# Kernel optimization log

Hardware: AMD Instinct MI355X
Metric: run time of the kernel (lower is better)

## Reference

```python
import jax, jax.numpy as jnp
import numpy as np

N = 50000; E = 800000; B = 500; L = 42
F_IN = 35; HEADS = 10; F_H = 35; F_G = 350
VOCAB = 26; EMB = 128; NF = 16; OUT_DIM = 128; K = 8
NEG_SLOPE = 0.2


def setup_inputs() -> dict:
    key = jax.random.key(0)
    ks = jax.random.split(key, 16)
    inp = {}
    inp['x'] = jax.random.normal(ks[0], (N, F_IN), jnp.float32)
    inp['edge_index'] = jax.random.randint(ks[1], (2, E), 0, N, dtype=jnp.int32)
    inp['batch'] = jnp.sort(jax.random.randint(ks[2], (N,), 0, B, dtype=jnp.int32))
    inp['target'] = jax.random.randint(ks[3], (B, L), 0, VOCAB, dtype=jnp.int32)
    # --- learned parameters ---
    inp['W_gat'] = jax.random.normal(ks[4], (F_IN, HEADS * F_H), jnp.float32) * 0.1
    inp['att_src'] = jax.random.normal(ks[5], (HEADS, F_H), jnp.float32) * 0.1
    inp['att_dst'] = jax.random.normal(ks[6], (HEADS, F_H), jnp.float32) * 0.1
    inp['b_gat'] = jnp.zeros((HEADS * F_H,), jnp.float32)
    inp['W_gcn'] = jax.random.normal(ks[7], (F_G, F_G), jnp.float32) * 0.05
    inp['b_gcn'] = jnp.zeros((F_G,), jnp.float32)
    inp['W_fcg1'] = jax.random.normal(ks[8], (2 * F_G, 1500), jnp.float32) * 0.03
    inp['b_fcg1'] = jnp.zeros((1500,), jnp.float32)
    inp['W_fcg2'] = jax.random.normal(ks[9], (1500, OUT_DIM), jnp.float32) * 0.03
    inp['b_fcg2'] = jnp.zeros((OUT_DIM,), jnp.float32)
    inp['emb_xt'] = jax.random.normal(ks[10], (VOCAB, EMB), jnp.float32) * 0.1
    inp['W_conv'] = jax.random.normal(ks[11], (NF, EMB, K), jnp.float32) * 0.05
    inp['b_conv'] = jnp.zeros((NF,), jnp.float32)
    inp['W_fcxt'] = jax.random.normal(ks[12], (NF * 35, OUT_DIM), jnp.float32) * 0.05
    inp['b_fcxt'] = jnp.zeros((OUT_DIM,), jnp.float32)
    inp['W_fc1'] = jax.random.normal(ks[13], (256, 512), jnp.float32) * 0.05
    inp['b_fc1'] = jnp.zeros((512,), jnp.float32)
    inp['W_out'] = jax.random.normal(ks[14], (512, 1), jnp.float32) * 0.05
    inp['b_out'] = jnp.zeros((1,), jnp.float32)
    return inp


def _add_self_loops(edge_index):
    loop = jnp.arange(N, dtype=edge_index.dtype)
    src = jnp.concatenate([edge_index[0], loop])
    dst = jnp.concatenate([edge_index[1], loop])
    return src, dst


def _gat_conv(x, src, dst, W, att_src, att_dst, b):
    # h: [N, H, C]
    h = (x @ W).reshape(N, HEADS, F_H)
    a_s = jnp.einsum('nhc,hc->nh', h, att_src)  # [N, H]
    a_d = jnp.einsum('nhc,hc->nh', h, att_dst)
    e = jax.nn.leaky_relu(a_s[src] + a_d[dst], NEG_SLOPE)  # [Etot, H]
    # segment softmax over incoming edges per destination node, per head
    m = jax.ops.segment_max(e, dst, num_segments=N)
    m = jnp.where(jnp.isfinite(m), m, 0.0)
    ex = jnp.exp(e - m[dst])
    den = jax.ops.segment_sum(ex, dst, num_segments=N)
    alpha = ex / (den[dst] + 1e-16)  # [Etot, H]
    out = jax.ops.segment_sum(h[src] * alpha[:, :, None], dst, num_segments=N)
    return out.reshape(N, HEADS * F_H) + b, alpha


def _gcn_conv(x, src, dst, W, b):
    deg = jax.ops.segment_sum(jnp.ones_like(dst, jnp.float32), dst, num_segments=N)
    dinv = jnp.where(deg > 0, deg ** -0.5, 0.0)
    norm = dinv[src] * dinv[dst]  # symmetric normalization
    h = x @ W
    return jax.ops.segment_sum(h[src] * norm[:, None], dst, num_segments=N) + b


def reference(x, edge_index, batch, target, W_gat, att_src, att_dst, b_gat,
              W_gcn, b_gcn, W_fcg1, b_fcg1, W_fcg2, b_fcg2, emb_xt,
              W_conv, b_conv, W_fcxt, b_fcxt, W_fc1, b_fc1, W_out, b_out):
    src, dst = _add_self_loops(edge_index)
    # --- graph branch ---
    xg, alpha = _gat_conv(x, src, dst, W_gat, att_src, att_dst, b_gat)
    xg = jax.nn.relu(xg)
    xg = jax.nn.relu(_gcn_conv(xg, src, dst, W_gcn, b_gcn))
    # global max + mean pool per graph
    gmax = jax.ops.segment_max(xg, batch, num_segments=B)
    gsum = jax.ops.segment_sum(xg, batch, num_segments=B)
    cnt = jax.ops.segment_sum(jnp.ones((N,), jnp.float32), batch, num_segments=B)
    gmean = gsum / jnp.maximum(cnt, 1.0)[:, None]
    xg = jnp.concatenate([gmax, gmean], axis=1)  # [B, 700]
    xg = jax.nn.relu(xg @ W_fcg1 + b_fcg1)
    xg = xg @ W_fcg2 + b_fcg2  # [B, 128] (dropout is identity in eval)
    # --- protein branch ---
    emb = emb_xt[target]                      # [B, L, 128]
    emb = jnp.transpose(emb, (0, 2, 1))       # [B, 128, L]
    conv = jax.lax.conv_general_dilated(
        emb, W_conv, window_strides=(1,), padding='VALID',
        dimension_numbers=('NCH', 'OIH', 'NCH'))  # [B, 16, 35]
    conv = conv + b_conv[None, :, None]
    xt = conv.reshape(B, NF * 35)
    xt = xt @ W_fcxt + b_fcxt                 # [B, 128]
    # --- fusion ---
    xc = jnp.concatenate([xg, xt], axis=1)    # [B, 256]
    xc = jax.nn.relu(xc @ W_fc1 + b_fc1)
    out = jax.nn.sigmoid(xc @ W_out + b_out)  # [B, 1]
    return out, alpha
```

## Files before the change

### kernel.cpp

```cpp
#include <hip/hip_runtime.h>
#include <math.h>

#define NN 50000
#define EE 800000
#define BB 500
#define LL 42
#define NHEAD 10
#define FH 35
#define FG 350
#define ETOT (EE + NN)
#define NCHUNK ((NN + 511) / 512)

#define KPAD 384
#define MPAD 50048
#define MB2  512

typedef unsigned short ushort_t;
typedef __attribute__((ext_vector_type(8))) short short8v;
typedef __attribute__((ext_vector_type(4))) float float4v;

__device__ __forceinline__ float lrelu(float x) { return x > 0.f ? x : 0.2f * x; }

__device__ __forceinline__ ushort_t f2bf(float f) {
    unsigned int u = __float_as_uint(f);
    u += 0x7fffu + ((u >> 16) & 1u);
    return (ushort_t)(u >> 16);
}
__device__ __forceinline__ float bflo(unsigned u) { return __uint_as_float(u << 16); }
__device__ __forceinline__ float bfhi(unsigned u) { return __uint_as_float(u & 0xffff0000u); }
__device__ __forceinline__ unsigned packbf(float a, float b) {
    return (unsigned)f2bf(a) | ((unsigned)f2bf(b) << 16);
}

__device__ __forceinline__ void async_cp16(const void* g, void* l) {
    __builtin_amdgcn_global_load_lds((const __attribute__((address_space(1))) unsigned int*)g,
                                     (__attribute__((address_space(3))) unsigned int*)l, 16, 0, 0);
}

__global__ __launch_bounds__(256) void k_init(int* deg, int* cur) {
    int i = blockIdx.x * 256 + threadIdx.x;
    if (i < NN) { deg[i] = 1; cur[i] = 0; }
}

__global__ __launch_bounds__(256) void k_deg(const int* __restrict__ ei, int* deg) {
    int i = blockIdx.x * 256 + threadIdx.x;
    if (i < EE) atomicAdd(&deg[ei[EE + i]], 1);
}

__global__ __launch_bounds__(512) void k_scan1(const int* __restrict__ deg, int* part) {
    int i = blockIdx.x * 512 + threadIdx.x;
    int lane = threadIdx.x & 63, wv = threadIdx.x >> 6;
    int x = (i < NN) ? deg[i] : 0;
    #pragma unroll
    for (int d = 32; d; d >>= 1) x += __shfl_xor(x, d);
    __shared__ int wsum[8];
    if (lane == 0) wsum[wv] = x;
    __syncthreads();
    if (threadIdx.x == 0) {
        int s = 0;
        #pragma unroll
        for (int w = 0; w < 8; w++) s += wsum[w];
        part[blockIdx.x] = s;
    }
}

__global__ __launch_bounds__(64) void k_scan2(const int* __restrict__ part, int* pscan) {
    int l = threadIdx.x;
    int v0 = (l < NCHUNK) ? part[l] : 0;
    #pragma unroll
    for (int d = 1; d < 64; d <<= 1) { int t = __shfl_up(v0, d); if (l >= d) v0 += t; }
    int tot0 = __shfl(v0, 63);
    int v1 = (64 + l < NCHUNK) ? part[64 + l] : 0;
    #pragma unroll
    for (int d = 1; d < 64; d <<= 1) { int t = __shfl_up(v1, d); if (l >= d) v1 += t; }
    v1 += tot0;
    if (l < NCHUNK) pscan[l] = v0;
    if (64 + l < NCHUNK) pscan[64 + l] = v1;
}

__global__ __launch_bounds__(512) void k_scan3(const int* __restrict__ deg, const int* __restrict__ pscan,
                                               int* offs) {
    int i = blockIdx.x * 512 + threadIdx.x;
    int lane = threadIdx.x & 63, wv = threadIdx.x >> 6;
    int x = (i < NN) ? deg[i] : 0;
    int incl = x;
    #pragma unroll
    for (int d = 1; d < 64; d <<= 1) { int t = __shfl_up(incl, d); if (lane >= d) incl += t; }
    __shared__ int wtot[8];
    if (lane == 63) wtot[wv] = incl;
    __syncthreads();
    int woff = 0;
    for (int w = 0; w < wv; w++) woff += wtot[w];
    int base = (blockIdx.x == 0) ? 0 : pscan[blockIdx.x - 1];
    if (i < NN) offs[i] = base + woff + incl - x;
}

__global__ __launch_bounds__(256) void k_scatter(const int* __restrict__ ei, const int* __restrict__ offs,
                                                 int* cur, int* csr_src) {
    int i = blockIdx.x * 256 + threadIdx.x;
    if (i < EE) {
        int s = ei[i], d = ei[EE + i];
        int slot = atomicAdd(&cur[d], 1);
        csr_src[offs[d] + slot] = s;
    } else if (i < ETOT) {
        int v = i - EE;
        int slot = atomicAdd(&cur[v], 1);
        csr_src[offs[v] + slot] = v;
    }
}

__global__ __launch_bounds__(256) void k_dinv(const int* __restrict__ deg, float* dinv) {
    int i = blockIdx.x * 256 + threadIdx.x;
    if (i < NN) dinv[i] = rsqrtf((float)deg[i]);
}

__global__ __launch_bounds__(256) void k_prep_x(const float* __restrict__ x, ushort_t* __restrict__ xb) {
    int i = blockIdx.x * 256 + threadIdx.x;
    if (i >= MPAD * 64) return;
    int r = i / 64, k = i % 64;
    float v = (r < NN && k < 35) ? x[r * 35 + k] : 0.f;
    xb[i] = f2bf(v);
}

__global__ __launch_bounds__(256) void k_prep_wgat(const float* __restrict__ W, ushort_t* __restrict__ Wt) {
    int i = blockIdx.x * 256 + threadIdx.x;
    if (i >= KPAD * 64) return;
    int n = i / 64, k = i % 64;
    float v = (n < FG && k < 35) ? W[k * FG + n] : 0.f;
    Wt[i] = f2bf(v);
}

__global__ __launch_bounds__(256) void k_prep_wgcn(const float* __restrict__ W, ushort_t* __restrict__ Wt) {
    int i = blockIdx.x * 256 + threadIdx.x;
    if (i >= KPAD * KPAD) return;
    int n = i / KPAD, k = i % KPAD;
    float v = (n < FG && k < FG) ? W[k * FG + n] : 0.f;
    Wt[i] = f2bf(v);
}

__global__ __launch_bounds__(256) void k_prep_w(const float* __restrict__ W, ushort_t* __restrict__ Wt,
                                                int K, int N, int KP, int NP) {
    int i = blockIdx.x * 256 + threadIdx.x;
    if (i >= KP * NP) return;
    int k = i / NP, n = i % NP;
    float v = (k < K && n < N) ? W[(size_t)k * N + n] : 0.f;
    Wt[(size_t)n * KP + k] = f2bf(v);
}

__global__ __launch_bounds__(256) void k_cast_pad(const float* __restrict__ src, ushort_t* __restrict__ dst,
                                                  int M, int K, int MP, int KP) {
    int i = blockIdx.x * 256 + threadIdx.x;
    if (i >= MP * KP) return;
    int r = i / KP, k = i % KP;
    dst[i] = (r < M && k < K) ? f2bf(src[(size_t)r * K + k]) : (ushort_t)0;
}

__global__ __launch_bounds__(256) void k_zero_tail(ushort_t* xg1b) {
    int i = blockIdx.x * 256 + threadIdx.x;
    int total = (MPAD - NN) * KPAD;
    if (i < total) xg1b[(size_t)NN * KPAD + i] = 0;
}

__global__ __launch_bounds__(256) void k_mfma(const ushort_t* __restrict__ A, const ushort_t* __restrict__ Bt,
                                              void* __restrict__ C, int M, int Nv, int ldc, int lda,
                                              int ksteps, const float* __restrict__ bias, int act, int bf16out) {
    __shared__ ushort_t As[128 * 64];
    __shared__ ushort_t Bs[64 * 64];
    int tid = threadIdx.x;
    int wid = tid >> 6, lane = tid & 63;
    int m0 = blockIdx.y * 128, n0 = blockIdx.x * 64;
    int wm0 = (wid >> 1) * 64, wn0 = (wid & 1) * 32;
    int srow = tid >> 3;
    int scol = (tid & 7) * 8;
    float4v acc[4][2] = {{{0.f,0.f,0.f,0.f},{0.f,0.f,0.f,0.f}},
                         {{0.f,0.f,0.f,0.f},{0.f,0.f,0.f,0.f}},
                         {{0.f,0.f,0.f,0.f},{0.f,0.f,0.f,0.f}},
                         {{0.f,0.f,0.f,0.f},{0.f,0.f,0.f,0.f}}};
    int a_off = (wm0 + (lane & 15)) * 64 + (lane >> 4) * 8;
    int b_off = (wn0 + (lane & 15)) * 64 + (lane >> 4) * 8;
    for (int ks = 0; ks < ksteps; ks++) {
        int k0 = ks * 64;
        #pragma unroll
        for (int r = 0; r < 4; r++) {
            const ushort_t* g = A + (size_t)(m0 + r * 32 + srow) * lda + k0 + scol;
            async_cp16(g, As + (r * 256 + tid) * 8);
        }
        #pragma unroll
        for (int r = 0; r < 2; r++) {
            const ushort_t* g = Bt + (size_t)(n0 + r * 32 + srow) * lda + k0 + scol;
            async_cp16(g, Bs + (r * 256 + tid) * 8);
        }
        __syncthreads();
        #pragma unroll
        for (int kh = 0; kh < 2; kh++) {
            short8v b0 = *(const short8v*)&Bs[b_off + kh * 32];
            short8v b1 = *(const short8v*)&Bs[b_off + 16 * 64 + kh * 32];
            #pragma unroll
            for (int mi = 0; mi < 4; mi++) {
                short8v a = *(const short8v*)&As[a_off + mi * 16 * 64 + kh * 32];
                acc[mi][0] = __builtin_amdgcn_mfma_f32_16x16x32_bf16(a, b0, acc[mi][0], 0, 0, 0);
                acc[mi][1] = __builtin_amdgcn_mfma_f32_16x16x32_bf16(a, b1, acc[mi][1], 0, 0, 0);
            }
        }
        __syncthreads();
    }
    int lm = m0 + wm0 + (lane >> 4) * 4;
    int lc = n0 + wn0 + (lane & 15);
    #pragma unroll
    for (int mi = 0; mi < 4; mi++) {
        #pragma unroll
        for (int ni = 0; ni < 2; ni++) {
            int col = lc + ni * 16;
            float bv = (bias != nullptr && col < Nv) ? bias[col] : 0.f;
            #pragma unroll
            for (int r = 0; r < 4; r++) {
                int row = lm + mi * 16 + r;
                if (row >= M) continue;
                float v = acc[mi][ni][r] + bv;
                if (act) v = fmaxf(v, 0.f);
                if (col >= Nv) v = 0.f;
                if (bf16out) ((ushort_t*)C)[(size_t)row * ldc + col] = f2bf(v);
                else         ((float*)C)[(size_t)row * ldc + col] = v;
            }
        }
    }
}

__global__ __launch_bounds__(256) void k_att(const ushort_t* __restrict__ hb, const float* __restrict__ att_s,
                                             const float* __restrict__ att_d, float* __restrict__ a_s,
                                             float* __restrict__ a_d) {
    int tid = blockIdx.x * 256 + threadIdx.x;
    if (tid >= NN * NHEAD) return;
    int n = tid / NHEAD, hd = tid % NHEAD;
    const ushort_t* hr = hb + (size_t)n * KPAD + hd * FH;
    const float* ws = att_s + hd * FH;
    const float* wd = att_d + hd * FH;
    float as = 0.f, ad = 0.f;
    #pragma unroll
    for (int c = 0; c < FH; c++) {
        float v = __uint_as_float(((unsigned)hr[c]) << 16);
        as += v * ws[c]; ad += v * wd[c];
    }
    a_s[tid] = as;
    a_d[tid] = ad;
}

__global__ __launch_bounds__(256) void k_gat_agg(const ushort_t* __restrict__ hb, const float* __restrict__ a_s,
                                                 const float* __restrict__ a_d,
                                                 const int* __restrict__ csr_src,
                                                 const int* __restrict__ offs, const int* __restrict__ deg,
                                                 const float* __restrict__ b_gat,
                                                 ushort_t* __restrict__ xg1b, float* __restrict__ denArr) {
    int wid = (blockIdx.x * blockDim.x + threadIdx.x) >> 6;
    int lane = threadIdx.x & 63;
    if (wid >= NN) return;
    int o0 = offs[wid], d = deg[wid];
    bool mine = (lane < NHEAD);
    float adv = mine ? a_d[wid * NHEAD + lane] : 0.f;
    int hA0 = (2 * lane) / 35,       hA1 = (2 * lane + 1) / 35;
    int hB0 = (128 + 2 * lane) / 35, hB1 = (129 + 2 * lane) / 35;
    int hC0 = (256 + 2 * lane) / 35, hC1 = (257 + 2 * lane) / 35;
    float den = 0.f;
    float aL0 = 0.f, aH0 = 0.f, aL1 = 0.f, aH1 = 0.f, aL2 = 0.f, aH2 = 0.f;
    const unsigned* hb32 = (const unsigned*)hb;
    int i = 0;
    for (; i + 2 <= d; i += 2) {
        int s0 = csr_src[o0 + i], s1 = csr_src[o0 + i + 1];
        float as0 = mine ? a_s[s0 * NHEAD + lane] : 0.f;
        float as1 = mine ? a_s[s1 * NHEAD + lane] : 0.f;
        const unsigned* h0 = hb32 + (size_t)s0 * (KPAD / 2);
        const unsigned* h1 = hb32 + (size_t)s1 * (KPAD / 2);
        unsigned u00 = h0[lane], u01 = h0[lane + 64], u02 = h0[lane + 128];
        unsigned u10 = h1[lane], u11 = h1[lane + 64], u12 = h1[lane + 128];
        float ex0 = __expf(lrelu(as0 + adv));
        float ex1 = __expf(lrelu(as1 + adv));
        den += ex0 + ex1;
        aL0 += __shfl(ex0, hA0) * bflo(u00) + __shfl(ex1, hA0) * bflo(u10);
        aH0 += __shfl(ex0, hA1) * bfhi(u00) + __shfl(ex1, hA1) * bfhi(u10);
        aL1 += __shfl(ex0, hB0) * bflo(u01) + __shfl(ex1, hB0) * bflo(u11);
        aH1 += __shfl(ex0, hB1) * bfhi(u01) + __shfl(ex1, hB1) * bfhi(u11);
        aL2 += __shfl(ex0, hC0) * bflo(u02) + __shfl(ex1, hC0) * bflo(u12);
        aH2 += __shfl(ex0, hC1) * bfhi(u02) + __shfl(ex1, hC1) * bfhi(u12);
    }
    for (; i < d; i++) {
        int s = csr_src[o0 + i];
        float asv = mine ? a_s[s * NHEAD + lane] : 0.f;
        float ex = __expf(lrelu(asv + adv));
        den += ex;
        const unsigned* hr = hb32 + (size_t)s * (KPAD / 2);
        unsigned u0 = hr[lane], u1 = hr[lane + 64], u2 = hr[lane + 128];
        aL0 += __shfl(ex, hA0) * bflo(u0);  aH0 += __shfl(ex, hA1) * bfhi(u0);
        aL1 += __shfl(ex, hB0) * bflo(u1);  aH1 += __shfl(ex, hB1) * bfhi(u1);
        aL2 += __shfl(ex, hC0) * bflo(u2);  aH2 += __shfl(ex, hC1) * bfhi(u2);
    }
    float rden = 1.f / (den + 1e-16f);
    if (mine) denArr[wid * NHEAD + lane] = den;
    unsigned* orow = (unsigned*)(xg1b + (size_t)wid * KPAD);
    {
        int f = 2 * lane;
        float v0 = fmaxf(aL0 * __shfl(rden, hA0) + b_gat[f], 0.f);
        float v1 = fmaxf(aH0 * __shfl(rden, hA1) + b_gat[f + 1], 0.f);
        orow[lane] = packbf(v0, v1);
    }
    {
        int f = 128 + 2 * lane;
        float v0 = fmaxf(aL1 * __shfl(rden, hB0) + b_gat[f], 0.f);
        float v1 = fmaxf(aH1 * __shfl(rden, hB1) + b_gat[f + 1], 0.f);
        orow[lane + 64] = packbf(v0, v1);
    }
    {
        int f = 256 + 2 * lane;
        unsigned pv = 0;
        if (f < FG) {
            float v0 = fmaxf(aL2 * __shfl(rden, hC0) + b_gat[f], 0.f);
            float v1 = fmaxf(aH2 * __shfl(rden, hC1) + b_gat[f + 1], 0.f);
            pv = packbf(v0, v1);
        }
        orow[lane + 128] = pv;
    }
}

__global__ __launch_bounds__(256) void k_alpha(const int* __restrict__ ei, const float* __restrict__ a_s,
                                               const float* __restrict__ a_d, const float* __restrict__ den,
                                               float* __restrict__ alphaOut) {
    int i = blockIdx.x * 256 + threadIdx.x;
    if (i >= ETOT * NHEAD) return;
    int e = i / NHEAD, hd = i % NHEAD;
    int s, dst;
    if (e < EE) { s = ei[e]; dst = ei[EE + e]; }
    else { s = dst = e - EE; }
    float ex = __expf(lrelu(a_s[s * NHEAD + hd] + a_d[dst * NHEAD + hd]));
    alphaOut[i] = ex / (den[dst * NHEAD + hd] + 1e-16f);
}

__global__ __launch_bounds__(256) void k_gcn_agg(const ushort_t* __restrict__ h2b,
                                                 const int* __restrict__ csr_src,
                                                 const int* __restrict__ offs, const int* __restrict__ deg,
                                                 const float* __restrict__ dinv, const float* __restrict__ b_gcn,
                                                 float* __restrict__ xg2) {
    int wid = (blockIdx.x * blockDim.x + threadIdx.x) >> 6;
    int lane = threadIdx.x & 63;
    if (wid >= NN) return;
    int o0 = offs[wid], d = deg[wid];
    float wv = dinv[wid];
    float aL0 = 0.f, aH0 = 0.f, aL1 = 0.f, aH1 = 0.f, aL2 = 0.f, aH2 = 0.f;
    const unsigned* h32 = (const unsigned*)h2b;
    int i = 0;
    for (; i + 2 <= d; i += 2) {
        int s0 = csr_src[o0 + i], s1 = csr_src[o0 + i + 1];
        float w0 = dinv[s0], w1 = dinv[s1];
        const unsigned* h0 = h32 + (size_t)s0 * (KPAD / 2);
        const unsigned* h1 = h32 + (size_t)s1 * (KPAD / 2);
        unsigned u00 = h0[lane], u01 = h0[lane + 64], u02 = h0[lane + 128];
        unsigned u10 = h1[lane], u11 = h1[lane + 64], u12 = h1[lane + 128];
        aL0 += w0 * bflo(u00) + w1 * bflo(u10);
        aH0 += w0 * bfhi(u00) + w1 * bfhi(u10);
        aL1 += w0 * bflo(u01) + w1 * bflo(u11);
        aH1 += w0 * bfhi(u01) + w1 * bfhi(u11);
        aL2 += w0 * bflo(u02) + w1 * bflo(u12);
        aH2 += w0 * bfhi(u02) + w1 * bfhi(u12);
    }
    for (; i < d; i++) {
        int s = csr_src[o0 + i];
        float ws = dinv[s];
        const unsigned* hr = h32 + (size_t)s * (KPAD / 2);
        unsigned u0 = hr[lane], u1 = hr[lane + 64], u2 = hr[lane + 128];
        aL0 += ws * bflo(u0);  aH0 += ws * bfhi(u0);
        aL1 += ws * bflo(u1);  aH1 += ws * bfhi(u1);
        aL2 += ws * bflo(u2);  aH2 += ws * bfhi(u2);
    }
    float* orow = xg2 + (size_t)wid * FG;
    {
        int f = 2 * lane;
        float2 v = { fmaxf(wv * aL0 + b_gcn[f], 0.f), fmaxf(wv * aH0 + b_gcn[f + 1], 0.f) };
        *(float2*)&orow[f] = v;
    }
    {
        int f = 128 + 2 * lane;
        float2 v = { fmaxf(wv * aL1 + b_gcn[f], 0.f), fmaxf(wv * aH1 + b_gcn[f + 1], 0.f) };
        *(float2*)&orow[f] = v;
    }
    {
        int f = 256 + 2 * lane;
        if (f < FG) {
            float2 v = { fmaxf(wv * aL2 + b_gcn[f], 0.f), fmaxf(wv * aH2 + b_gcn[f + 1], 0.f) };
            *(float2*)&orow[f] = v;
        }
    }
}

__device__ __forceinline__ int lowerB(const int* a, int n, int key) {
    int lo = 0, hi = n;
    while (lo < hi) { int mid = (lo + hi) >> 1; if (a[mid] < key) lo = mid + 1; else hi = mid; }
    return lo;
}

__global__ __launch_bounds__(384) void k_pool(const float* __restrict__ xg2, const int* __restrict__ batch,
                                              float* __restrict__ pooled) {
    int g = blockIdx.x;
    int f = threadIdx.x;
    int s = lowerB(batch, NN, g);
    int e = lowerB(batch, NN, g + 1);
    if (f >= FG) return;
    float mx = -INFINITY, sm = 0.f;
    for (int n = s; n < e; n++) {
        float v = xg2[(size_t)n * FG + f];
        mx = fmaxf(mx, v);
        sm += v;
    }
    int cnt = e - s;
    pooled[g * 700 + f] = mx;
    pooled[g * 700 + FG + f] = sm / fmaxf((float)cnt, 1.f);
}

__global__ __launch_bounds__(256) void k_conv(const int* __restrict__ target, const float* __restrict__ emb,
                                              const float* __restrict__ Wc, const float* __restrict__ bc,
                                              float* __restrict__ xt) {
    __shared__ float embL[26 * 132];
    __shared__ float WL[16 * 8 * 128];
    __shared__ int   tgL[2 * LL];
    int tid = threadIdx.x;
    int b0 = blockIdx.x * 2;
    for (int i = tid; i < 26 * 128; i += 256) {
        int r = i >> 7, e = i & 127;
        embL[r * 132 + e] = emb[i];
    }
    for (int i = tid; i < 16384; i += 256) {
        int f = i >> 10, rem = i & 1023, k = rem >> 7, e = rem & 127;
        WL[i] = Wc[f * 1024 + e * 8 + k];
    }
    if (tid < 2 * LL) tgL[tid] = target[b0 * LL + tid];
    __syncthreads();
    #pragma unroll
    for (int pass = 0; pass < 2; pass++) {
        int r = tid + pass * 256;
        if (r >= 280) break;
        int bl = r / 140, rem = r % 140;
        int fq = rem / 35, t = rem % 35;
        const int* tg = &tgL[bl * LL];
        float ac0 = 0.f, ac1 = 0.f, ac2 = 0.f, ac3 = 0.f;
        for (int k = 0; k < 8; k++) {
            const float* er = &embL[tg[t + k] * 132];
            const float* w0 = &WL[((fq * 4 + 0) * 8 + k) * 128];
            const float* w1 = &WL[((fq * 4 + 1) * 8 + k) * 128];
            const float* w2 = &WL[((fq * 4 + 2) * 8 + k) * 128];
            const float* w3 = &WL[((fq * 4 + 3) * 8 + k) * 128];
            #pragma unroll 8
            for (int e = 0; e < 128; e += 4) {
                float4 a = *(const float4*)&er[e];
                float4 q0 = *(const float4*)&w0[e];
                float4 q1 = *(const float4*)&w1[e];
                float4 q2 = *(const float4*)&w2[e];
                float4 q3 = *(const float4*)&w3[e];
                ac0 += a.x * q0.x + a.y * q0.y + a.z * q0.z + a.w * q0.w;
                ac1 += a.x * q1.x + a.y * q1.y + a.z * q1.z + a.w * q1.w;
                ac2 += a.x * q2.x + a.y * q2.y + a.z * q2.z + a.w * q2.w;
                ac3 += a.x * q3.x + a.y * q3.y + a.z * q3.z + a.w * q3.w;
            }
        }
        int b = b0 + bl, fb = fq * 4;
        xt[b * 560 + (fb + 0) * 35 + t] = ac0 + bc[fb + 0];
        xt[b * 560 + (fb + 1) * 35 + t] = ac1 + bc[fb + 1];
        xt[b * 560 + (fb + 2) * 35 + t] = ac2 + bc[fb + 2];
        xt[b * 560 + (fb + 3) * 35 + t] = ac3 + bc[fb + 3];
    }
}

__global__ __launch_bounds__(256) void k_out(const float* __restrict__ f1, const float* __restrict__ W_out,
                                             const float* __restrict__ b_out, float* __restrict__ out) {
    int wid = (blockIdx.x * blockDim.x + threadIdx.x) >> 6;
    int lane = threadIdx.x & 63;
    if (wid >= BB) return;
    const float* xr = f1 + (size_t)wid * 512;
    float acc = 0.f;
    #pragma unroll
    for (int k = 0; k < 8; k++) acc += xr[lane + k * 64] * W_out[lane + k * 64];
    #pragma unroll
    for (int d = 32; d; d >>= 1) acc += __shfl_xor(acc, d);
    if (lane == 0) out[wid] = 1.f / (1.f + __expf(-(acc + b_out[0])));
}

extern "C" void kernel_launch(void* const* d_in, const int* in_sizes, int n_in,
                              void* d_out, int out_size, void* d_ws, size_t ws_size,
                              hipStream_t stream) {
    const float* x      = (const float*)d_in[0];
    const int*   ei     = (const int*)d_in[1];
    const int*   batch  = (const int*)d_in[2];
    const int*   target = (const int*)d_in[3];
    const float* W_gat  = (const float*)d_in[4];
    const float* att_s  = (const float*)d_in[5];
    const float* att_d  = (const float*)d_in[6];
    const float* b_gat  = (const float*)d_in[7];
    const float* W_gcn  = (const float*)d_in[8];
    const float* b_gcn  = (const float*)d_in[9];
    const float* W_fcg1 = (const float*)d_in[10];
    const float* b_fcg1 = (const float*)d_in[11];
    const float* W_fcg2 = (const float*)d_in[12];
    const float* b_fcg2 = (const float*)d_in[13];
    const float* embxt  = (const float*)d_in[14];
    const float* W_conv = (const float*)d_in[15];
    const float* b_conv = (const float*)d_in[16];
    const float* W_fcxt = (const float*)d_in[17];
    const float* b_fcxt = (const float*)d_in[18];
    const float* W_fc1  = (const float*)d_in[19];
    const float* b_fc1  = (const float*)d_in[20];
    const float* W_out  = (const float*)d_in[21];
    const float* b_out  = (const float*)d_in[22];

    float* out_sig  = (float*)d_out;
    float* alphaOut = (float*)d_out + BB;

    size_t o = 0;
    auto alloc = [&](size_t bytes) -> void* {
        o = (o + 255) & ~(size_t)255;
        void* p = (char*)d_ws + o;
        o += bytes;
        return p;
    };
    int*   deg     = (int*)alloc((size_t)NN * 4);
    int*   cur     = (int*)alloc((size_t)NN * 4);
    int*   offs    = (int*)alloc((size_t)NN * 4);
    int*   part    = (int*)alloc(128 * 4);
    int*   pscan   = (int*)alloc(128 * 4);
    int*   csr_src = (int*)alloc((size_t)ETOT * 4);
    float* dinv    = (float*)alloc((size_t)NN * 4);
    float* a_s     = (float*)alloc((size_t)NN * NHEAD * 4);
    float* a_d     = (float*)alloc((size_t)NN * NHEAD * 4);
    float* denArr  = (float*)alloc((size_t)NN * NHEAD * 4);
    ushort_t* xb16 = (ushort_t*)alloc((size_t)MPAD * 64 * 2);
    ushort_t* WtGA = (ushort_t*)alloc((size_t)KPAD * 64 * 2);
    ushort_t* WtGC = (ushort_t*)alloc((size_t)KPAD * KPAD * 2);
    ushort_t* WtF1 = (ushort_t*)alloc((size_t)1536 * 704 * 2);
    ushort_t* WtF2 = (ushort_t*)alloc((size_t)128 * 1536 * 2);
    ushort_t* WtFX = (ushort_t*)alloc((size_t)128 * 576 * 2);
    ushort_t* WtFC = (ushort_t*)alloc((size_t)512 * 256 * 2);
    float* pooled  = (float*)alloc((size_t)BB * 700 * 4);
    ushort_t* pooledb = (ushort_t*)alloc((size_t)MB2 * 704 * 2);
    ushort_t* t1b  = (ushort_t*)alloc((size_t)MB2 * 1536 * 2);
    float* xt      = (float*)alloc((size_t)BB * 560 * 4);
    ushort_t* xtb  = (ushort_t*)alloc((size_t)MB2 * 576 * 2);
    ushort_t* xcb  = (ushort_t*)alloc((size_t)MB2 * 256 * 2);
    float* f1      = (float*)alloc((size_t)MB2 * 512 * 4);
    ushort_t* hb   = (ushort_t*)alloc((size_t)MPAD * KPAD * 2);
    char*  R2      = (char*)alloc((size_t)NN * FG * 4);
    ushort_t* xg1b = (ushort_t*)R2;
    float* xg2     = (float*)R2;
    (void)ws_size; (void)n_in; (void)in_sizes; (void)out_size;

    auto mfma = [&](const ushort_t* A, const ushort_t* Bt, void* C, const float* bias,
                    int M2, int Nv, int NP, int ldc, int KP, int act, int bf16out) {
        dim3 g(NP / 64, M2 / 128);
        k_mfma<<<g, 256, 0, stream>>>(A, Bt, C, M2, Nv, ldc, KP, KP / 64, bias, act, bf16out);
    };

    k_init<<<(NN + 255) / 256, 256, 0, stream>>>(deg, cur);
    k_deg<<<(EE + 255) / 256, 256, 0, stream>>>(ei, deg);
    k_scan1<<<NCHUNK, 512, 0, stream>>>(deg, part);
    k_scan2<<<1, 64, 0, stream>>>(part, pscan);
    k_scan3<<<NCHUNK, 512, 0, stream>>>(deg, pscan, offs);
    k_scatter<<<(ETOT + 255) / 256, 256, 0, stream>>>(ei, offs, cur, csr_src);
    k_dinv<<<(NN + 255) / 256, 256, 0, stream>>>(deg, dinv);

    k_prep_x<<<(MPAD * 64 + 255) / 256, 256, 0, stream>>>(x, xb16);
    k_prep_wgat<<<(KPAD * 64 + 255) / 256, 256, 0, stream>>>(W_gat, WtGA);
    k_prep_wgcn<<<(KPAD * KPAD + 255) / 256, 256, 0, stream>>>(W_gcn, WtGC);
    k_prep_w<<<(704 * 1536 + 255) / 256, 256, 0, stream>>>(W_fcg1, WtF1, 700, 1500, 704, 1536);
    k_prep_w<<<(1536 * 128 + 255) / 256, 256, 0, stream>>>(W_fcg2, WtF2, 1500, 128, 1536, 128);
    k_prep_w<<<(576 * 128 + 255) / 256, 256, 0, stream>>>(W_fcxt, WtFX, 560, 128, 576, 128);
    k_prep_w<<<(256 * 512 + 255) / 256, 256, 0, stream>>>(W_fc1, WtFC, 256, 512, 256, 512);
    k_zero_tail<<<((MPAD - NN) * KPAD + 255) / 256, 256, 0, stream>>>(xg1b);

    mfma(xb16, WtGA, hb, nullptr, MPAD, KPAD, KPAD, KPAD, 64, 0, 1);
    k_att<<<(NN * NHEAD + 255) / 256, 256, 0, stream>>>(hb, att_s, att_d, a_s, a_d);
    k_gat_agg<<<(NN + 3) / 4, 256, 0, stream>>>(hb, a_s, a_d, csr_src, offs, deg, b_gat, xg1b, denArr);
    k_alpha<<<(ETOT * NHEAD + 255) / 256, 256, 0, stream>>>(ei, a_s, a_d, denArr, alphaOut);

    mfma(xg1b, WtGC, hb, nullptr, MPAD, KPAD, KPAD, KPAD, KPAD, 0, 1);
    k_gcn_agg<<<(NN + 3) / 4, 256, 0, stream>>>(hb, csr_src, offs, deg, dinv, b_gcn, xg2);

    k_pool<<<BB, 384, 0, stream>>>(xg2, batch, pooled);
    k_cast_pad<<<(MB2 * 704 + 255) / 256, 256, 0, stream>>>(pooled, pooledb, BB, 700, MB2, 704);
    mfma(pooledb, WtF1, t1b, b_fcg1, MB2, 1500, 1536, 1536, 704, 1, 1);
    mfma(t1b, WtF2, xcb, b_fcg2, MB2, 128, 128, 256, 1536, 0, 1);
    k_conv<<<250, 256, 0, stream>>>(target, embxt, W_conv, b_conv, xt);
    k_cast_pad<<<(MB2 * 576 + 255) / 256, 256, 0, stream>>>(xt, xtb, BB, 560, MB2, 576);
    mfma(xtb, WtFX, xcb + 128, b_fcxt, MB2, 128, 128, 256, 576, 0, 1);
    mfma(xcb, WtFC, f1, b_fc1, MB2, 512, 512, 512, 256, 1, 0);
    k_out<<<(BB + 3) / 4, 256, 0, stream>>>(f1, W_out, b_out, out_sig);
}
```

Measured before the change: 628.0 us.

## Aggregate raw inputs before GAT projection using block-diagonal weight matmul

The GAT attention logits are now computed directly from x using precomputed W·att vectors. Aggregation gathers the 35-wide fp32 input rows per head instead of the 350-wide projected bf16 rows, shrinking per-edge gather traffic. The head-wise projection, bias and ReLU are then applied afterwards with a block-diagonal MFMA GEMM that skips zero K-blocks. The pooling loop is also unrolled by four. The trade-off is that per-head aggregated inputs still produce a 350-wide write plus an extra GEMM, and the pad rows of xg1b are no longer explicitly zeroed.

```diff
diff --git a/kernel.cpp b/kernel.cpp
--- a/kernel.cpp
+++ b/kernel.cpp
@@ -28,9 +28,6 @@
 }
 __device__ __forceinline__ float bflo(unsigned u) { return __uint_as_float(u << 16); }
 __device__ __forceinline__ float bfhi(unsigned u) { return __uint_as_float(u & 0xffff0000u); }
-__device__ __forceinline__ unsigned packbf(float a, float b) {
-    return (unsigned)f2bf(a) | ((unsigned)f2bf(b) << 16);
-}
 
 __device__ __forceinline__ void async_cp16(const void* g, void* l) {
     __builtin_amdgcn_global_load_lds((const __attribute__((address_space(1))) unsigned int*)g,
@@ -114,19 +111,35 @@
     if (i < NN) dinv[i] = rsqrtf((float)deg[i]);
 }
 
-__global__ __launch_bounds__(256) void k_prep_x(const float* __restrict__ x, ushort_t* __restrict__ xb) {
-    int i = blockIdx.x * 256 + threadIdx.x;
-    if (i >= MPAD * 64) return;
-    int r = i / 64, k = i % 64;
-    float v = (r < NN && k < 35) ? x[r * 35 + k] : 0.f;
-    xb[i] = f2bf(v);
-}
-
-__global__ __launch_bounds__(256) void k_prep_wgat(const float* __restrict__ W, ushort_t* __restrict__ Wt) {
-    int i = blockIdx.x * 256 + threadIdx.x;
-    if (i >= KPAD * 64) return;
-    int n = i / 64, k = i % 64;
-    float v = (n < FG && k < 35) ? W[k * FG + n] : 0.f;
+__global__ __launch_bounds__(256) void k_prep_xf(const float* __restrict__ x, float* __restrict__ xf) {
+    int i = blockIdx.x * 256 + threadIdx.x;
+    if (i >= NN * 40) return;
+    int n = i / 40, c = i % 40;
+    xf[i] = (c < 35) ? x[n * 35 + c] : 0.f;
+}
+
+__global__ __launch_bounds__(256) void k_prep_att(const float* __restrict__ W_gat, const float* __restrict__ att_s,
+                                                  const float* __restrict__ att_d,
+                                                  float* __restrict__ wS, float* __restrict__ wD) {
+    int i = blockIdx.x * 256 + threadIdx.x;
+    if (i >= FG) return;
+    int hd = i / 35, c = i % 35;
+    float ss = 0.f, dd = 0.f;
+    for (int cc = 0; cc < 35; cc++) {
+        float w = W_gat[c * FG + hd * 35 + cc];
+        ss += w * att_s[hd * 35 + cc];
+        dd += w * att_d[hd * 35 + cc];
+    }
+    wS[i] = ss;
+    wD[i] = dd;
+}
+
+__global__ __launch_bounds__(256) void k_prep_wbd(const float* __restrict__ W_gat, ushort_t* __restrict__ Wt) {
+    int i = blockIdx.x * 256 + threadIdx.x;
+    if (i >= KPAD * KPAD) return;
+    int n = i / KPAD, k = i % KPAD;
+    float v = 0.f;
+    if (n < FG && k < FG && (k / 35) == (n / 35)) v = W_gat[(k % 35) * FG + n];
     Wt[i] = f2bf(v);
 }
 
@@ -155,15 +168,10 @@
     dst[i] = (r < M && k < K) ? f2bf(src[(size_t)r * K + k]) : (ushort_t)0;
 }
 
-__global__ __launch_bounds__(256) void k_zero_tail(ushort_t* xg1b) {
-    int i = blockIdx.x * 256 + threadIdx.x;
-    int total = (MPAD - NN) * KPAD;
-    if (i < total) xg1b[(size_t)NN * KPAD + i] = 0;
-}
-
 __global__ __launch_bounds__(256) void k_mfma(const ushort_t* __restrict__ A, const ushort_t* __restrict__ Bt,
                                               void* __restrict__ C, int M, int Nv, int ldc, int lda,
-                                              int ksteps, const float* __restrict__ bias, int act, int bf16out) {
+                                              int ksteps, const float* __restrict__ bias, int act, int bf16out,
+                                              int bdiag) {
     __shared__ ushort_t As[128 * 64];
     __shared__ ushort_t Bs[64 * 64];
     int tid = threadIdx.x;
@@ -178,7 +186,14 @@
                          {{0.f,0.f,0.f,0.f},{0.f,0.f,0.f,0.f}}};
     int a_off = (wm0 + (lane & 15)) * 64 + (lane >> 4) * 8;
     int b_off = (wn0 + (lane & 15)) * 64 + (lane >> 4) * 8;
-    for (int ks = 0; ks < ksteps; ks++) {
+    int ks0 = 0, ks1 = ksteps;
+    if (bdiag) {
+        int hlo = n0 / 35;
+        int hhi = (n0 + 63) / 35; if (hhi > 9) hhi = 9;
+        ks0 = (hlo * 35) >> 6;
+        ks1 = ((hhi + 1) * 35 + 63) >> 6;
+    }
+    for (int ks = ks0; ks < ks1; ks++) {
         int k0 = ks * 64;
         #pragma unroll
         for (int r = 0; r < 4; r++) {
@@ -226,98 +241,79 @@
     }
 }
 
-__global__ __launch_bounds__(256) void k_att(const ushort_t* __restrict__ hb, const float* __restrict__ att_s,
-                                             const float* __restrict__ att_d, float* __restrict__ a_s,
-                                             float* __restrict__ a_d) {
+__global__ __launch_bounds__(256) void k_att2(const float* __restrict__ x, const float* __restrict__ wS,
+                                              const float* __restrict__ wD, float* __restrict__ a_s,
+                                              float* __restrict__ a_d) {
     int tid = blockIdx.x * 256 + threadIdx.x;
     if (tid >= NN * NHEAD) return;
     int n = tid / NHEAD, hd = tid % NHEAD;
-    const ushort_t* hr = hb + (size_t)n * KPAD + hd * FH;
-    const float* ws = att_s + hd * FH;
-    const float* wd = att_d + hd * FH;
+    const float* xr = x + (size_t)n * 35;
+    const float* ws = wS + hd * 35;
+    const float* wd = wD + hd * 35;
     float as = 0.f, ad = 0.f;
     #pragma unroll
-    for (int c = 0; c < FH; c++) {
-        float v = __uint_as_float(((unsigned)hr[c]) << 16);
-        as += v * ws[c]; ad += v * wd[c];
-    }
+    for (int c = 0; c < 35; c++) { float v = xr[c]; as += v * ws[c]; ad += v * wd[c]; }
     a_s[tid] = as;
     a_d[tid] = ad;
 }
 
-__global__ __launch_bounds__(256) void k_gat_agg(const ushort_t* __restrict__ hb, const float* __restrict__ a_s,
+__global__ __launch_bounds__(256) void k_gat_agg(const float* __restrict__ xf, const float* __restrict__ a_s,
                                                  const float* __restrict__ a_d,
                                                  const int* __restrict__ csr_src,
                                                  const int* __restrict__ offs, const int* __restrict__ deg,
-                                                 const float* __restrict__ b_gat,
-                                                 ushort_t* __restrict__ xg1b, float* __restrict__ denArr) {
+                                                 ushort_t* __restrict__ Zb, float* __restrict__ denArr) {
     int wid = (blockIdx.x * blockDim.x + threadIdx.x) >> 6;
     int lane = threadIdx.x & 63;
     if (wid >= NN) return;
     int o0 = offs[wid], d = deg[wid];
     bool mine = (lane < NHEAD);
     float adv = mine ? a_d[wid * NHEAD + lane] : 0.f;
-    int hA0 = (2 * lane) / 35,       hA1 = (2 * lane + 1) / 35;
-    int hB0 = (128 + 2 * lane) / 35, hB1 = (129 + 2 * lane) / 35;
-    int hC0 = (256 + 2 * lane) / 35, hC1 = (257 + 2 * lane) / 35;
+    int f0 = lane, f1 = lane + 64, f2 = lane + 128, f3 = lane + 192, f4 = lane + 256, f5 = lane + 320;
+    int h0 = f0 / 35, h1 = f1 / 35, h2 = f2 / 35, h3 = f3 / 35, h4 = f4 / 35;
+    int h5 = (f5 < FG) ? f5 / 35 : 0;
+    int c0 = f0 % 35, c1 = f1 % 35, c2 = f2 % 35, c3 = f3 % 35, c4 = f4 % 35;
+    int c5 = (f5 < FG) ? f5 % 35 : 0;
     float den = 0.f;
-    float aL0 = 0.f, aH0 = 0.f, aL1 = 0.f, aH1 = 0.f, aL2 = 0.f, aH2 = 0.f;
-    const unsigned* hb32 = (const unsigned*)hb;
+    float ac0 = 0.f, ac1 = 0.f, ac2 = 0.f, ac3 = 0.f, ac4 = 0.f, ac5 = 0.f;
     int i = 0;
     for (; i + 2 <= d; i += 2) {
         int s0 = csr_src[o0 + i], s1 = csr_src[o0 + i + 1];
+        const float* x0 = xf + (size_t)s0 * 40;
+        const float* x1 = xf + (size_t)s1 * 40;
         float as0 = mine ? a_s[s0 * NHEAD + lane] : 0.f;
         float as1 = mine ? a_s[s1 * NHEAD + lane] : 0.f;
-        const unsigned* h0 = hb32 + (size_t)s0 * (KPAD / 2);
-        const unsigned* h1 = hb32 + (size_t)s1 * (KPAD / 2);
-        unsigned u00 = h0[lane], u01 = h0[lane + 64], u02 = h0[lane + 128];
-        unsigned u10 = h1[lane], u11 = h1[lane + 64], u12 = h1[lane + 128];
         float ex0 = __expf(lrelu(as0 + adv));
         float ex1 = __expf(lrelu(as1 + adv));
         den += ex0 + ex1;
-        aL0 += __shfl(ex0, hA0) * bflo(u00) + __shfl(ex1, hA0) * bflo(u10);
-        aH0 += __shfl(ex0, hA1) * bfhi(u00) + __shfl(ex1, hA1) * bfhi(u10);
-        aL1 += __shfl(ex0, hB0) * bflo(u01) + __shfl(ex1, hB0) * bflo(u11);
-        aH1 += __shfl(ex0, hB1) * bfhi(u01) + __shfl(ex1, hB1) * bfhi(u11);
-        aL2 += __shfl(ex0, hC0) * bflo(u02) + __shfl(ex1, hC0) * bflo(u12);
-        aH2 += __shfl(ex0, hC1) * bfhi(u02) + __shfl(ex1, hC1) * bfhi(u12);
+        ac0 += __shfl(ex0, h0) * x0[c0] + __shfl(ex1, h0) * x1[c0];
+        ac1 += __shfl(ex0, h1) * x0[c1] + __shfl(ex1, h1) * x1[c1];
+        ac2 += __shfl(ex0, h2) * x0[c2] + __shfl(ex1, h2) * x1[c2];
+        ac3 += __shfl(ex0, h3) * x0[c3] + __shfl(ex1, h3) * x1[c3];
+        ac4 += __shfl(ex0, h4) * x0[c4] + __shfl(ex1, h4) * x1[c4];
+        ac5 += __shfl(ex0, h5) * x0[c5] + __shfl(ex1, h5) * x1[c5];
     }
     for (; i < d; i++) {
         int s = csr_src[o0 + i];
+        const float* xr = xf + (size_t)s * 40;
         float asv = mine ? a_s[s * NHEAD + lane] : 0.f;
         float ex = __expf(lrelu(asv + adv));
         den += ex;
-        const unsigned* hr = hb32 + (size_t)s * (KPAD / 2);
-        unsigned u0 = hr[lane], u1 = hr[lane + 64], u2 = hr[lane + 128];
-        aL0 += __shfl(ex, hA0) * bflo(u0);  aH0 += __shfl(ex, hA1) * bfhi(u0);
-        aL1 += __shfl(ex, hB0) * bflo(u1);  aH1 += __shfl(ex, hB1) * bfhi(u1);
-        aL2 += __shfl(ex, hC0) * bflo(u2);  aH2 += __shfl(ex, hC1) * bfhi(u2);
+        ac0 += __shfl(ex, h0) * xr[c0];
+        ac1 += __shfl(ex, h1) * xr[c1];
+        ac2 += __shfl(ex, h2) * xr[c2];
+        ac3 += __shfl(ex, h3) * xr[c3];
+        ac4 += __shfl(ex, h4) * xr[c4];
+        ac5 += __shfl(ex, h5) * xr[c5];
     }
     float rden = 1.f / (den + 1e-16f);
     if (mine) denArr[wid * NHEAD + lane] = den;
-    unsigned* orow = (unsigned*)(xg1b + (size_t)wid * KPAD);
-    {
-        int f = 2 * lane;
-        float v0 = fmaxf(aL0 * __shfl(rden, hA0) + b_gat[f], 0.f);
-        float v1 = fmaxf(aH0 * __shfl(rden, hA1) + b_gat[f + 1], 0.f);
-        orow[lane] = packbf(v0, v1);
-    }
-    {
-        int f = 128 + 2 * lane;
-        float v0 = fmaxf(aL1 * __shfl(rden, hB0) + b_gat[f], 0.f);
-        float v1 = fmaxf(aH1 * __shfl(rden, hB1) + b_gat[f + 1], 0.f);
-        orow[lane + 64] = packbf(v0, v1);
-    }
-    {
-        int f = 256 + 2 * lane;
-        unsigned pv = 0;
-        if (f < FG) {
-            float v0 = fmaxf(aL2 * __shfl(rden, hC0) + b_gat[f], 0.f);
-            float v1 = fmaxf(aH2 * __shfl(rden, hC1) + b_gat[f + 1], 0.f);
-            pv = packbf(v0, v1);
-        }
-        orow[lane + 128] = pv;
-    }
+    ushort_t* zr = Zb + (size_t)wid * KPAD;
+    zr[f0] = f2bf(ac0 * __shfl(rden, h0));
+    zr[f1] = f2bf(ac1 * __shfl(rden, h1));
+    zr[f2] = f2bf(ac2 * __shfl(rden, h2));
+    zr[f3] = f2bf(ac3 * __shfl(rden, h3));
+    zr[f4] = f2bf(ac4 * __shfl(rden, h4));
+    zr[f5] = (f5 < FG) ? f2bf(ac5 * __shfl(rden, h5)) : (ushort_t)0;
 }
 
 __global__ __launch_bounds__(256) void k_alpha(const int* __restrict__ ei, const float* __restrict__ a_s,
@@ -403,7 +399,16 @@
     int e = lowerB(batch, NN, g + 1);
     if (f >= FG) return;
     float mx = -INFINITY, sm = 0.f;
-    for (int n = s; n < e; n++) {
+    int n = s;
+    for (; n + 4 <= e; n += 4) {
+        float v0 = xg2[(size_t)(n + 0) * FG + f];
+        float v1 = xg2[(size_t)(n + 1) * FG + f];
+        float v2 = xg2[(size_t)(n + 2) * FG + f];
+        float v3 = xg2[(size_t)(n + 3) * FG + f];
+        mx = fmaxf(fmaxf(mx, v0), fmaxf(fmaxf(v1, v2), v3));
+        sm += v0 + v1 + v2 + v3;
+    }
+    for (; n < e; n++) {
         float v = xg2[(size_t)n * FG + f];
         mx = fmaxf(mx, v);
         sm += v;
@@ -527,8 +532,10 @@
     float* a_s     = (float*)alloc((size_t)NN * NHEAD * 4);
     float* a_d     = (float*)alloc((size_t)NN * NHEAD * 4);
     float* denArr  = (float*)alloc((size_t)NN * NHEAD * 4);
-    ushort_t* xb16 = (ushort_t*)alloc((size_t)MPAD * 64 * 2);
-    ushort_t* WtGA = (ushort_t*)alloc((size_t)KPAD * 64 * 2);
+    float* xf      = (float*)alloc((size_t)NN * 40 * 4);
+    float* wS      = (float*)alloc((size_t)FG * 4);
+    float* wD      = (float*)alloc((size_t)FG * 4);
+    ushort_t* WtBD = (ushort_t*)alloc((size_t)KPAD * KPAD * 2);
     ushort_t* WtGC = (ushort_t*)alloc((size_t)KPAD * KPAD * 2);
     ushort_t* WtF1 = (ushort_t*)alloc((size_t)1536 * 704 * 2);
     ushort_t* WtF2 = (ushort_t*)alloc((size_t)128 * 1536 * 2);
@@ -548,9 +555,9 @@
     (void)ws_size; (void)n_in; (void)in_sizes; (void)out_size;
 
     auto mfma = [&](const ushort_t* A, const ushort_t* Bt, void* C, const float* bias,
-                    int M2, int Nv, int NP, int ldc, int KP, int act, int bf16out) {
+                    int M2, int Nv, int NP, int ldc, int KP, int act, int bf16out, int bdiag) {
         dim3 g(NP / 64, M2 / 128);
-        k_mfma<<<g, 256, 0, stream>>>(A, Bt, C, M2, Nv, ldc, KP, KP / 64, bias, act, bf16out);
+        k_mfma<<<g, 256, 0, stream>>>(A, Bt, C, M2, Nv, ldc, KP, KP / 64, bias, act, bf16out, bdiag);
     };
 
     k_init<<<(NN + 255) / 256, 256, 0, stream>>>(deg, cur);
@@ -561,30 +568,30 @@
     k_scatter<<<(ETOT + 255) / 256, 256, 0, stream>>>(ei, offs, cur, csr_src);
     k_dinv<<<(NN + 255) / 256, 256, 0, stream>>>(deg, dinv);
 
-    k_prep_x<<<(MPAD * 64 + 255) / 256, 256, 0, stream>>>(x, xb16);
-    k_prep_wgat<<<(KPAD * 64 + 255) / 256, 256, 0, stream>>>(W_gat, WtGA);
+    k_prep_xf<<<(NN * 40 + 255) / 256, 256, 0, stream>>>(x, xf);
+    k_prep_att<<<2, 256, 0, stream>>>(W_gat, att_s, att_d, wS, wD);
+    k_prep_wbd<<<(KPAD * KPAD + 255) / 256, 256, 0, stream>>>(W_gat, WtBD);
     k_prep_wgcn<<<(KPAD * KPAD + 255) / 256, 256, 0, stream>>>(W_gcn, WtGC);
     k_prep_w<<<(704 * 1536 + 255) / 256, 256, 0, stream>>>(W_fcg1, WtF1, 700, 1500, 704, 1536);
     k_prep_w<<<(1536 * 128 + 255) / 256, 256, 0, stream>>>(W_fcg2, WtF2, 1500, 128, 1536, 128);
     k_prep_w<<<(576 * 128 + 255) / 256, 256, 0, stream>>>(W_fcxt, WtFX, 560, 128, 576, 128);
     k_prep_w<<<(256 * 512 + 255) / 256, 256, 0, stream>>>(W_fc1, WtFC, 256, 512, 256, 512);
-    k_zero_tail<<<((MPAD - NN) * KPAD + 255) / 256, 256, 0, stream>>>(xg1b);
-
-    mfma(xb16, WtGA, hb, nullptr, MPAD, KPAD, KPAD, KPAD, 64, 0, 1);
-    k_att<<<(NN * NHEAD + 255) / 256, 256, 0, stream>>>(hb, att_s, att_d, a_s, a_d);
-    k_gat_agg<<<(NN + 3) / 4, 256, 0, stream>>>(hb, a_s, a_d, csr_src, offs, deg, b_gat, xg1b, denArr);
+
+    k_att2<<<(NN * NHEAD + 255) / 256, 256, 0, stream>>>(x, wS, wD, a_s, a_d);
+    k_gat_agg<<<(NN + 3) / 4, 256, 0, stream>>>(xf, a_s, a_d, csr_src, offs, deg, hb, denArr);
     k_alpha<<<(ETOT * NHEAD + 255) / 256, 256, 0, stream>>>(ei, a_s, a_d, denArr, alphaOut);
-
-    mfma(xg1b, WtGC, hb, nullptr, MPAD, KPAD, KPAD, KPAD, KPAD, 0, 1);
+    mfma(hb, WtBD, xg1b, b_gat, MPAD, FG, KPAD, KPAD, KPAD, 1, 1, 1);
+
+    mfma(xg1b, WtGC, hb, nullptr, MPAD, KPAD, KPAD, KPAD, KPAD, 0, 1, 0);
     k_gcn_agg<<<(NN + 3) / 4, 256, 0, stream>>>(hb, csr_src, offs, deg, dinv, b_gcn, xg2);
 
     k_pool<<<BB, 384, 0, stream>>>(xg2, batch, pooled);
     k_cast_pad<<<(MB2 * 704 + 255) / 256, 256, 0, stream>>>(pooled, pooledb, BB, 700, MB2, 704);
-    mfma(pooledb, WtF1, t1b, b_fcg1, MB2, 1500, 1536, 1536, 704, 1, 1);
-    mfma(t1b, WtF2, xcb, b_fcg2, MB2, 128, 128, 256, 1536, 0, 1);
+    mfma(pooledb, WtF1, t1b, b_fcg1, MB2, 1500, 1536, 1536, 704, 1, 1, 0);
+    mfma(t1b, WtF2, xcb, b_fcg2, MB2, 128, 128, 256, 1536, 0, 1, 0);
     k_conv<<<250, 256, 0, stream>>>(target, embxt, W_conv, b_conv, xt);
     k_cast_pad<<<(MB2 * 576 + 255) / 256, 256, 0, stream>>>(xt, xtb, BB, 560, MB2, 576);
-    mfma(xtb, WtFX, xcb + 128, b_fcxt, MB2, 128, 128, 256, 576, 0, 1);
-    mfma(xcb, WtFC, f1, b_fc1, MB2, 512, 512, 512, 256, 1, 0);
+    mfma(xtb, WtFX, xcb + 128, b_fcxt, MB2, 128, 128, 256, 576, 0, 1, 0);
+    mfma(xcb, WtFC, f1, b_fc1, MB2, 512, 512, 512, 256, 1, 0, 0);
     k_out<<<(BB + 3) / 4, 256, 0, stream>>>(f1, W_out, b_out, out_sig);
 }
```

Result: slower. 645.5 us (+2.8%).
